# Kernel optimization log

Measured on AMD Instinct MI355X. Metric: run time of the kernel, lower is better.

The kernel has to match this reference:

```python
import jax, jax.numpy as jnp
import numpy as np

B, L, D, H = 2, 2048, 1024, 16
HD = D // H


def setup_inputs() -> dict:
    key = jax.random.key(0)
    ks = jax.random.split(key, 13)
    s = 0.02
    return {
        "x": jax.random.normal(ks[0], (B, L, D), jnp.float32),
        "pos_emb": jax.random.normal(ks[1], (1, L, D), jnp.float32),
        "Wq": jax.random.normal(ks[2], (D, D), jnp.float32) * s,
        "bq": jax.random.normal(ks[3], (D,), jnp.float32) * s,
        "Wk": jax.random.normal(ks[4], (D, D), jnp.float32) * s,
        "bk": jax.random.normal(ks[5], (D,), jnp.float32) * s,
        "Wv": jax.random.normal(ks[6], (D, D), jnp.float32) * s,
        "bv": jax.random.normal(ks[7], (D,), jnp.float32) * s,
        "Wpos": jax.random.normal(ks[8], (D, D), jnp.float32) * s,
        "pos_bias_u": jax.random.normal(ks[9], (H, HD), jnp.float32) * s,
        "pos_bias_v": jax.random.normal(ks[10], (H, HD), jnp.float32) * s,
        "Wo": jax.random.normal(ks[11], (D, D), jnp.float32) * s,
        "bo": jax.random.normal(ks[12], (D,), jnp.float32) * s,
    }


def _rel_shift(x):
    # x: (b, h, L, L) -> Transformer-XL relative shift
    b, h, q, k = x.shape
    x = jnp.pad(x, ((0, 0), (0, 0), (0, 0), (1, 0)))  # (b,h,L,L+1)
    x = x.reshape(b, h, k + 1, q)                      # (b,h,L+1,L)
    return x[:, :, 1:, :]                              # (b,h,L,L)


def reference(x, pos_emb, Wq, bq, Wk, bk, Wv, bv, Wpos, pos_bias_u, pos_bias_v, Wo, bo):
    b, seq, d = x.shape
    h, hd = pos_bias_u.shape
    scale = hd ** (-0.5)

    def proj(inp, W, bias=None):
        y = inp @ W.T
        if bias is not None:
            y = y + bias
        return y.reshape(inp.shape[0], seq, h, hd).transpose(0, 2, 1, 3)

    q = proj(x, Wq, bq)            # (b,h,L,hd)
    k = proj(x, Wk, bk)
    v = proj(x, Wv, bv)
    p = proj(pos_emb, Wpos)        # (1,h,L,hd)

    q_u = q + pos_bias_u[None, :, None, :]
    ac = jnp.einsum("bhqd,bhkd->bhqk", q_u, k)
    q_v = q + pos_bias_v[None, :, None, :]
    bd = jnp.matmul(q_v, jnp.swapaxes(p, -1, -2))  # broadcasts over batch
    bd = _rel_shift(bd)

    attn = jax.nn.softmax((ac + bd) * scale, axis=-1)
    out = jnp.einsum("bhqk,bhkd->bhqd", attn, v)
    out = out.transpose(0, 2, 1, 3).reshape(b, seq, d)
    return out @ Wo.T + bo
```

## Files before the change

### kernel.cpp

```cpp
#include <hip/hip_runtime.h>
#include <hip/hip_bf16.h>

constexpr int Lq = 2048;
constexpr int Dm = 1024;
constexpr int Hh = 16;
constexpr int HD = 64;

typedef __bf16 v8bf __attribute__((ext_vector_type(8)));
typedef short  v4s  __attribute__((ext_vector_type(4)));
typedef float  v4f  __attribute__((ext_vector_type(4)));

#define DEV static __device__ __forceinline__

DEV short f2bf(float f) {
  return (short)__builtin_bit_cast(unsigned short, __float2bfloat16(f));
}

DEV v4f MFMA(v8bf a, v8bf b, v4f c) {
  return __builtin_amdgcn_mfma_f32_16x16x32_bf16(a, b, c, 0, 0, 0);
}

template<int CTRL>
DEV float dppf(float x) {
  return __builtin_bit_cast(float, __builtin_amdgcn_update_dpp(
      0, __builtin_bit_cast(int, x), CTRL, 0xF, 0xF, true));
}
DEV float rowmax16(float x) {
  x = fmaxf(x, dppf<0xB1>(x));
  x = fmaxf(x, dppf<0x4E>(x));
  x = fmaxf(x, dppf<0x141>(x));
  x = fmaxf(x, dppf<0x140>(x));
  return x;
}
DEV float rowsum16(float x) {
  x += dppf<0xB1>(x);
  x += dppf<0x4E>(x);
  x += dppf<0x141>(x);
  x += dppf<0x140>(x);
  return x;
}

DEV float bperm(int byteaddr, float x) {
  return __builtin_bit_cast(float,
      __builtin_amdgcn_ds_bpermute(byteaddr, __builtin_bit_cast(int, x)));
}

#if __has_builtin(__builtin_amdgcn_exp2f)
DEV float exp2g(float x) { return __builtin_amdgcn_exp2f(x); }
#else
DEV float exp2g(float x) { return exp2f(x); }
#endif

DEV v4s cvt4(float4 v) {
  v4s w; w[0] = f2bf(v.x); w[1] = f2bf(v.y); w[2] = f2bf(v.z); w[3] = f2bf(v.w);
  return w;
}

template<int MODE>
__launch_bounds__(256)
__global__ void gemm_bt(const void* __restrict__ Aptr,
                        const float* __restrict__ W,
                        const float* __restrict__ bias,
                        const float* __restrict__ ubias,
                        const float* __restrict__ vbias,
                        void* __restrict__ out0,
                        void* __restrict__ out1)
{
  __shared__ short As[64][72];
  __shared__ short Bs[64][72];

  const int tid  = threadIdx.x;
  const int lane = tid & 63;
  const int wave = tid >> 6;
  const int lr   = lane & 15;
  const int lg   = lane >> 4;
  const int row0 = blockIdx.y * 64;
  const int col0 = blockIdx.x * 64;
  const int wr   = (wave >> 1) * 32;
  const int wc   = (wave & 1) * 32;

  const int srow = tid >> 2;
  const int scol = (tid & 3) * 16;

  v4f acc[2][2] = {};

  for (int k0 = 0; k0 < Dm; k0 += 64) {
    __syncthreads();
    if (MODE == 4) {
      const short* A = (const short*)Aptr;
      *(v8bf*)(&As[srow][scol]) =
          *(const v8bf*)(A + (size_t)(row0 + srow) * Dm + k0 + scol);
      *(v8bf*)(&As[srow][scol + 8]) =
          *(const v8bf*)(A + (size_t)(row0 + srow) * Dm + k0 + scol + 8);
    } else {
      const float* A = (const float*)Aptr;
      #pragma unroll
      for (int i = 0; i < 4; ++i) {
        float4 v = *(const float4*)(A + (size_t)(row0 + srow) * Dm + k0 + scol + i * 4);
        *(v4s*)(&As[srow][scol + i * 4]) = cvt4(v);
      }
    }
    #pragma unroll
    for (int i = 0; i < 4; ++i) {
      float4 v = *(const float4*)(W + (size_t)(col0 + srow) * Dm + k0 + scol + i * 4);
      *(v4s*)(&Bs[srow][scol + i * 4]) = cvt4(v);
    }
    __syncthreads();

    #pragma unroll
    for (int kk = 0; kk < 2; ++kk) {
      v8bf af[2], bfr[2];
      #pragma unroll
      for (int sm = 0; sm < 2; ++sm)
        af[sm] = *(const v8bf*)(&As[wr + sm * 16 + lr][kk * 32 + lg * 8]);
      #pragma unroll
      for (int sn = 0; sn < 2; ++sn)
        bfr[sn] = *(const v8bf*)(&Bs[wc + sn * 16 + lr][kk * 32 + lg * 8]);
      #pragma unroll
      for (int sm = 0; sm < 2; ++sm)
        #pragma unroll
        for (int sn = 0; sn < 2; ++sn)
          acc[sm][sn] = MFMA(af[sm], bfr[sn], acc[sm][sn]);
    }
  }

  #pragma unroll
  for (int sm = 0; sm < 2; ++sm) {
    #pragma unroll
    for (int sn = 0; sn < 2; ++sn) {
      #pragma unroll
      for (int r = 0; r < 4; ++r) {
        int i = row0 + wr + sm * 16 + lg * 4 + r;
        int o = col0 + wc + sn * 16 + lr;
        float val = acc[sm][sn][r];
        if (MODE == 0) {
          val += bias[o];
          int b = i >> 11, l = i & 2047;
          int h = o >> 6,  hd = o & 63;
          size_t idx = (((size_t)(b * Hh + h)) * Lq + l) * HD + hd;
          ((short*)out0)[idx] = f2bf(val + ubias[o]);
          ((short*)out1)[idx] = f2bf(val + vbias[o]);
        } else if (MODE == 1) {
          val += bias[o];
          int b = i >> 11, l = i & 2047;
          int h = o >> 6,  hd = o & 63;
          size_t idx = (((size_t)(b * Hh + h)) * Lq + l) * HD + hd;
          ((short*)out0)[idx] = f2bf(val);
        } else if (MODE == 2) {
          val += bias[o];
          int b = i >> 11, l = i & 2047;
          int h = o >> 6,  hd = o & 63;
          size_t idx = (((size_t)(b * Hh + h)) * HD + hd) * Lq + l;
          ((short*)out0)[idx] = f2bf(val);
        } else if (MODE == 3) {
          int h = o >> 6, hd = o & 63;
          size_t idx = ((size_t)h * Lq + i) * HD + hd;
          ((short*)out0)[idx] = f2bf(val);
        } else {
          ((float*)out0)[(size_t)i * Dm + o] = val + bias[o];
        }
      }
    }
  }
}

__launch_bounds__(256)
__global__ void attn_kernel(const short* __restrict__ Qu,
                            const short* __restrict__ Qv,
                            const short* __restrict__ Kb,
                            const short* __restrict__ Vt,
                            const short* __restrict__ Pb,
                            short* __restrict__ AO)
{
  __shared__ short Ks[64][72];
  __shared__ short Vs[64][72];
  __shared__ short Ps[4][16][72];

  const int tid  = threadIdx.x;
  const int lane = tid & 63;
  const int wave = tid >> 6;
  const int lr   = lane & 15;
  const int lg   = lane >> 4;
  const int bh   = blockIdx.y;
  const int h    = bh & (Hh - 1);
  const int Q0   = blockIdx.x * 64;
  const int q0   = Q0 + wave * 16;

  const short* Qu_bh = Qu + (size_t)bh * Lq * HD;
  const short* Qv_bh = Qv + (size_t)bh * Lq * HD;
  const short* Kb_bh = Kb + (size_t)bh * Lq * HD;
  const short* Vt_bh = Vt + (size_t)bh * HD * Lq;
  const short* Pb_h  = Pb + (size_t)h * Lq * HD;

  int  addr4[4];
  bool hi4[4];
  #pragma unroll
  for (int r = 0; r < 4; ++r) {
    int c = lr - (lg * 4 + r) + 15;
    hi4[r]  = (c >= 16);
    addr4[r] = (((lane & 48) | (c & 15)) << 2);
  }

  v8bf qu[2], qv1[2], qv2[2];
  {
    int q  = q0 + lr;
    int q2 = (q + 1 < Lq) ? q + 1 : Lq - 1;
    #pragma unroll
    for (int kk = 0; kk < 2; ++kk) {
      qu[kk]  = *(const v8bf*)(Qu_bh + (size_t)q  * HD + kk * 32 + lg * 8);
      qv1[kk] = *(const v8bf*)(Qv_bh + (size_t)q  * HD + kk * 32 + lg * 8);
      qv2[kk] = *(const v8bf*)(Qv_bh + (size_t)q2 * HD + kk * 32 + lg * 8);
    }
  }

  const int srow = tid >> 2;
  const int scol = (tid & 3) * 16;

  v8bf kpre0 = *(const v8bf*)(Kb_bh + (size_t)srow * HD + scol);
  v8bf kpre1 = *(const v8bf*)(Kb_bh + (size_t)srow * HD + scol + 8);
  v8bf vpre0 = *(const v8bf*)(Vt_bh + (size_t)srow * Lq + scol);
  v8bf vpre1 = *(const v8bf*)(Vt_bh + (size_t)srow * Lq + scol + 8);

  float m_r[4], l_r[4];
  v4f o_acc[4];
  #pragma unroll
  for (int r = 0; r < 4; ++r) { m_r[r] = -1e30f; l_r[r] = 0.f; }
  #pragma unroll
  for (int n = 0; n < 4; ++n) o_acc[n] = v4f{0.f, 0.f, 0.f, 0.f};

  const float sc = 0.125f * 1.44269504088896f;

  for (int ktile = 0; ktile < Lq / 64; ++ktile) {
    const int k0 = ktile * 64;
    __syncthreads();
    *(v8bf*)(&Ks[srow][scol])     = kpre0;
    *(v8bf*)(&Ks[srow][scol + 8]) = kpre1;
    *(v8bf*)(&Vs[srow][scol])     = vpre0;
    *(v8bf*)(&Vs[srow][scol + 8]) = vpre1;
    __syncthreads();
    if (ktile + 1 < Lq / 64) {
      const int kn = k0 + 64;
      kpre0 = *(const v8bf*)(Kb_bh + (size_t)(kn + srow) * HD + scol);
      kpre1 = *(const v8bf*)(Kb_bh + (size_t)(kn + srow) * HD + scol + 8);
      vpre0 = *(const v8bf*)(Vt_bh + (size_t)srow * Lq + kn + scol);
      vpre1 = *(const v8bf*)(Vt_bh + (size_t)srow * Lq + kn + scol + 8);
    }

    v4f s[4];
    #pragma unroll
    for (int kt4 = 0; kt4 < 4; ++kt4) {
      v4f a = v4f{0.f, 0.f, 0.f, 0.f};
      #pragma unroll
      for (int kk = 0; kk < 2; ++kk) {
        v8bf kb = *(const v8bf*)(&Ks[kt4 * 16 + lr][kk * 32 + lg * 8]);
        a = MFMA(qu[kk], kb, a);
      }
      s[kt4] = a;
    }

    const int thr = q0 - k0 + 15;
    const bool needT1 = (thr >= 0);
    const bool needT2 = (thr <= 76);
    const int jb1 = 2032 + k0 - q0;
    const int jb2 = k0 - q0 - 17;
    v4f t1[5] = {}, t2[5] = {};
    if (needT1) {
      #pragma unroll
      for (int n = 0; n < 5; ++n) {
        if (n * 16 <= thr) {
          int j = jb1 + n * 16 + lr;
          j = j < 0 ? 0 : (j > Lq - 1 ? Lq - 1 : j);
          v4f a = v4f{0.f, 0.f, 0.f, 0.f};
          #pragma unroll
          for (int kk = 0; kk < 2; ++kk) {
            v8bf pb = *(const v8bf*)(Pb_h + (size_t)j * HD + kk * 32 + lg * 8);
            a = MFMA(qv1[kk], pb, a);
          }
          t1[n] = a;
        }
      }
    }
    if (needT2) {
      #pragma unroll
      for (int n = 0; n < 5; ++n) {
        if (n * 16 + 15 >= thr + 2) {
          int j = jb2 + n * 16 + lr;
          j = j < 0 ? 0 : (j > Lq - 1 ? Lq - 1 : j);
          v4f a = v4f{0.f, 0.f, 0.f, 0.f};
          #pragma unroll
          for (int kk = 0; kk < 2; ++kk) {
            v8bf pb = *(const v8bf*)(Pb_h + (size_t)j * HD + kk * 32 + lg * 8);
            a = MFMA(qv2[kk], pb, a);
          }
          t2[n] = a;
        }
      }
    }

    #pragma unroll
    for (int n = 0; n < 5; ++n) {
      int cc = n * 16 + lr;
      #pragma unroll
      for (int r = 0; r < 4; ++r) {
        float v = (cc <= thr) ? t1[n][r] : ((cc == thr + 1) ? 0.f : t2[n][r]);
        t1[n][r] = v;
      }
    }

    #pragma unroll
    for (int kt4 = 0; kt4 < 4; ++kt4) {
      #pragma unroll
      for (int r = 0; r < 4; ++r) {
        float va = bperm(addr4[r], t1[kt4][r]);
        float vb = bperm(addr4[r], t1[kt4 + 1][r]);
        float bd = hi4[r] ? vb : va;
        s[kt4][r] = (s[kt4][r] + bd) * sc;
      }
    }

    #pragma unroll
    for (int r = 0; r < 4; ++r) {
      float rmax = fmaxf(fmaxf(s[0][r], s[1][r]), fmaxf(s[2][r], s[3][r]));
      rmax = rowmax16(rmax);
      float mnew  = fmaxf(m_r[r], rmax);
      float alpha = exp2g(m_r[r] - mnew);
      m_r[r] = mnew;
      float rsum = 0.f;
      #pragma unroll
      for (int kt4 = 0; kt4 < 4; ++kt4) {
        float p = exp2g(s[kt4][r] - mnew);
        s[kt4][r] = p;
        rsum += p;
      }
      rsum = rowsum16(rsum);
      l_r[r] = l_r[r] * alpha + rsum;
      #pragma unroll
      for (int n = 0; n < 4; ++n)
        o_acc[n][r] = o_acc[n][r] * alpha;
      #pragma unroll
      for (int kt4 = 0; kt4 < 4; ++kt4)
        Ps[wave][lg * 4 + r][kt4 * 16 + lr] = f2bf(s[kt4][r]);
    }
    asm volatile("s_waitcnt lgkmcnt(0)" ::: "memory");
    __builtin_amdgcn_sched_barrier(0);

    #pragma unroll
    for (int kk = 0; kk < 2; ++kk) {
      v8bf pa = *(const v8bf*)(&Ps[wave][lr][kk * 32 + lg * 8]);
      #pragma unroll
      for (int n = 0; n < 4; ++n) {
        v8bf vb = *(const v8bf*)(&Vs[n * 16 + lr][kk * 32 + lg * 8]);
        o_acc[n] = MFMA(pa, vb, o_acc[n]);
      }
    }
  }

  const int b = bh >> 4;
  #pragma unroll
  for (int r = 0; r < 4; ++r) {
    float inv = 1.0f / l_r[r];
    int q = q0 + lg * 4 + r;
    #pragma unroll
    for (int n = 0; n < 4; ++n) {
      int hd = n * 16 + lr;
      AO[((size_t)b * Lq + q) * Dm + h * HD + hd] = f2bf(o_acc[n][r] * inv);
    }
  }
}

extern "C" void kernel_launch(void* const* d_in, const int* in_sizes, int n_in,
                              void* d_out, int out_size, void* d_ws, size_t ws_size,
                              hipStream_t stream)
{
  (void)in_sizes; (void)n_in; (void)out_size; (void)ws_size;
  const float* x    = (const float*)d_in[0];
  const float* pos  = (const float*)d_in[1];
  const float* Wq   = (const float*)d_in[2];
  const float* bq   = (const float*)d_in[3];
  const float* Wk   = (const float*)d_in[4];
  const float* bk   = (const float*)d_in[5];
  const float* Wv   = (const float*)d_in[6];
  const float* bv   = (const float*)d_in[7];
  const float* Wpos = (const float*)d_in[8];
  const float* pu   = (const float*)d_in[9];
  const float* pvb  = (const float*)d_in[10];
  const float* Wo   = (const float*)d_in[11];
  const float* bo   = (const float*)d_in[12];
  float* out = (float*)d_out;

  short* Qu = (short*)d_ws;
  short* Qv = Qu + (size_t)4 * 1024 * 1024;
  short* Kb = Qv + (size_t)4 * 1024 * 1024;
  short* Vt = Kb + (size_t)4 * 1024 * 1024;
  short* Pb = Vt + (size_t)4 * 1024 * 1024;
  short* AO = Pb + (size_t)2 * 1024 * 1024;

  dim3 blk(256);
  gemm_bt<0><<<dim3(16, 64), blk, 0, stream>>>(x,   Wq,   bq,      pu,      pvb,     Qu,  Qv);
  gemm_bt<1><<<dim3(16, 64), blk, 0, stream>>>(x,   Wk,   bk,      nullptr, nullptr, Kb,  nullptr);
  gemm_bt<2><<<dim3(16, 64), blk, 0, stream>>>(x,   Wv,   bv,      nullptr, nullptr, Vt,  nullptr);
  gemm_bt<3><<<dim3(16, 32), blk, 0, stream>>>(pos, Wpos, nullptr, nullptr, nullptr, Pb,  nullptr);
  attn_kernel<<<dim3(Lq / 64, 2 * Hh), blk, 0, stream>>>(Qu, Qv, Kb, Vt, Pb, AO);
  gemm_bt<4><<<dim3(16, 64), blk, 0, stream>>>(AO,  Wo,   bo,      nullptr, nullptr, out, nullptr);
}
```

Before: 397.0 us.

## Batch QKV/pos projections into one launch, pre-convert inputs, drop LDS staging in attention

Adds kernels that convert x and pos_emb to bf16 once, then merges the four projection GEMMs into a single 3D-grid launch with per-z epilogues. The attention kernel no longer stages K/V in shared memory and reads MFMA fragments straight from global memory. It fuses the band computation into the score loop and skips the online-softmax rescale when no row max increases. This aims to cut launch count, repeated fp32 conversion of x and block-wide syncs. The cost is uncoalesced global K/V reads that rely on cache hits, plus extra conversion passes.

Result: slower. 597.5 us (+50.5%).

```diff
diff --git a/kernel.cpp b/kernel.cpp
--- a/kernel.cpp
+++ b/kernel.cpp
@@ -56,15 +56,120 @@
   return w;
 }
 
-template<int MODE>
 __launch_bounds__(256)
-__global__ void gemm_bt(const void* __restrict__ Aptr,
-                        const float* __restrict__ W,
-                        const float* __restrict__ bias,
-                        const float* __restrict__ ubias,
-                        const float* __restrict__ vbias,
-                        void* __restrict__ out0,
-                        void* __restrict__ out1)
+__global__ void cvt_bf16(const float* __restrict__ in, short* __restrict__ out,
+                         int n8)
+{
+  int i = blockIdx.x * 256 + threadIdx.x;
+  if (i >= n8) return;
+  float4 a = *(const float4*)(in + (size_t)i * 8);
+  float4 b = *(const float4*)(in + (size_t)i * 8 + 4);
+  *(v4s*)(out + (size_t)i * 8)     = cvt4(a);
+  *(v4s*)(out + (size_t)i * 8 + 4) = cvt4(b);
+}
+
+__launch_bounds__(256)
+__global__ void gemm_qkvp(const short* __restrict__ xb,
+                          const short* __restrict__ posb,
+                          const float* __restrict__ Wq, const float* __restrict__ Wk,
+                          const float* __restrict__ Wv, const float* __restrict__ Wp,
+                          const float* __restrict__ bq, const float* __restrict__ bk,
+                          const float* __restrict__ bv,
+                          const float* __restrict__ pu, const float* __restrict__ pvb,
+                          short* __restrict__ Qu, short* __restrict__ Qv,
+                          short* __restrict__ Kb, short* __restrict__ Vt,
+                          short* __restrict__ Pb)
+{
+  const int z    = blockIdx.z;
+  const int row0 = blockIdx.y * 64;
+  const int col0 = blockIdx.x * 64;
+  if (z == 3 && row0 >= Lq) return;
+  const short* A = (z == 3) ? posb : xb;
+  const float* W = (z == 0) ? Wq : (z == 1) ? Wk : (z == 2) ? Wv : Wp;
+
+  __shared__ short As[64][72];
+  __shared__ short Bs[64][72];
+
+  const int tid  = threadIdx.x;
+  const int lane = tid & 63;
+  const int wave = tid >> 6;
+  const int lr   = lane & 15;
+  const int lg   = lane >> 4;
+  const int wr   = (wave >> 1) * 32;
+  const int wc   = (wave & 1) * 32;
+  const int srow = tid >> 2;
+  const int scol = (tid & 3) * 16;
+
+  v4f acc[2][2] = {};
+
+  for (int k0 = 0; k0 < Dm; k0 += 64) {
+    __syncthreads();
+    *(v8bf*)(&As[srow][scol]) =
+        *(const v8bf*)(A + (size_t)(row0 + srow) * Dm + k0 + scol);
+    *(v8bf*)(&As[srow][scol + 8]) =
+        *(const v8bf*)(A + (size_t)(row0 + srow) * Dm + k0 + scol + 8);
+    #pragma unroll
+    for (int i = 0; i < 4; ++i) {
+      float4 v = *(const float4*)(W + (size_t)(col0 + srow) * Dm + k0 + scol + i * 4);
+      *(v4s*)(&Bs[srow][scol + i * 4]) = cvt4(v);
+    }
+    __syncthreads();
+
+    #pragma unroll
+    for (int kk = 0; kk < 2; ++kk) {
+      v8bf af[2], bfr[2];
+      #pragma unroll
+      for (int sm = 0; sm < 2; ++sm)
+        af[sm] = *(const v8bf*)(&As[wr + sm * 16 + lr][kk * 32 + lg * 8]);
+      #pragma unroll
+      for (int sn = 0; sn < 2; ++sn)
+        bfr[sn] = *(const v8bf*)(&Bs[wc + sn * 16 + lr][kk * 32 + lg * 8]);
+      #pragma unroll
+      for (int sm = 0; sm < 2; ++sm)
+        #pragma unroll
+        for (int sn = 0; sn < 2; ++sn)
+          acc[sm][sn] = MFMA(af[sm], bfr[sn], acc[sm][sn]);
+    }
+  }
+
+  #pragma unroll
+  for (int sm = 0; sm < 2; ++sm) {
+    #pragma unroll
+    for (int sn = 0; sn < 2; ++sn) {
+      #pragma unroll
+      for (int r = 0; r < 4; ++r) {
+        int i = row0 + wr + sm * 16 + lg * 4 + r;
+        int o = col0 + wc + sn * 16 + lr;
+        float val = acc[sm][sn][r];
+        int b = i >> 11, l = i & 2047;
+        int hh = o >> 6, hd = o & 63;
+        if (z == 0) {
+          val += bq[o];
+          size_t idx = (((size_t)(b * Hh + hh)) * Lq + l) * HD + hd;
+          Qu[idx] = f2bf(val + pu[o]);
+          Qv[idx] = f2bf(val + pvb[o]);
+        } else if (z == 1) {
+          val += bk[o];
+          size_t idx = (((size_t)(b * Hh + hh)) * Lq + l) * HD + hd;
+          Kb[idx] = f2bf(val);
+        } else if (z == 2) {
+          val += bv[o];
+          size_t idx = (((size_t)(b * Hh + hh)) * HD + hd) * Lq + l;
+          Vt[idx] = f2bf(val);
+        } else {
+          size_t idx = ((size_t)hh * Lq + i) * HD + hd;
+          Pb[idx] = f2bf(val);
+        }
+      }
+    }
+  }
+}
+
+__launch_bounds__(256)
+__global__ void gemm_out(const short* __restrict__ A,
+                         const float* __restrict__ W,
+                         const float* __restrict__ bias,
+                         float* __restrict__ out)
 {
   __shared__ short As[64][72];
   __shared__ short Bs[64][72];
@@ -78,7 +183,6 @@
   const int col0 = blockIdx.x * 64;
   const int wr   = (wave >> 1) * 32;
   const int wc   = (wave & 1) * 32;
-
   const int srow = tid >> 2;
   const int scol = (tid & 3) * 16;
 
@@ -86,20 +190,10 @@
 
   for (int k0 = 0; k0 < Dm; k0 += 64) {
     __syncthreads();
-    if (MODE == 4) {
-      const short* A = (const short*)Aptr;
-      *(v8bf*)(&As[srow][scol]) =
-          *(const v8bf*)(A + (size_t)(row0 + srow) * Dm + k0 + scol);
-      *(v8bf*)(&As[srow][scol + 8]) =
-          *(const v8bf*)(A + (size_t)(row0 + srow) * Dm + k0 + scol + 8);
-    } else {
-      const float* A = (const float*)Aptr;
-      #pragma unroll
-      for (int i = 0; i < 4; ++i) {
-        float4 v = *(const float4*)(A + (size_t)(row0 + srow) * Dm + k0 + scol + i * 4);
-        *(v4s*)(&As[srow][scol + i * 4]) = cvt4(v);
-      }
-    }
+    *(v8bf*)(&As[srow][scol]) =
+        *(const v8bf*)(A + (size_t)(row0 + srow) * Dm + k0 + scol);
+    *(v8bf*)(&As[srow][scol + 8]) =
+        *(const v8bf*)(A + (size_t)(row0 + srow) * Dm + k0 + scol + 8);
     #pragma unroll
     for (int i = 0; i < 4; ++i) {
       float4 v = *(const float4*)(W + (size_t)(col0 + srow) * Dm + k0 + scol + i * 4);
@@ -125,43 +219,15 @@
   }
 
   #pragma unroll
-  for (int sm = 0; sm < 2; ++sm) {
-    #pragma unroll
-    for (int sn = 0; sn < 2; ++sn) {
+  for (int sm = 0; sm < 2; ++sm)
+    #pragma unroll
+    for (int sn = 0; sn < 2; ++sn)
       #pragma unroll
       for (int r = 0; r < 4; ++r) {
         int i = row0 + wr + sm * 16 + lg * 4 + r;
         int o = col0 + wc + sn * 16 + lr;
-        float val = acc[sm][sn][r];
-        if (MODE == 0) {
-          val += bias[o];
-          int b = i >> 11, l = i & 2047;
-          int h = o >> 6,  hd = o & 63;
-          size_t idx = (((size_t)(b * Hh + h)) * Lq + l) * HD + hd;
-          ((short*)out0)[idx] = f2bf(val + ubias[o]);
-          ((short*)out1)[idx] = f2bf(val + vbias[o]);
-        } else if (MODE == 1) {
-          val += bias[o];
-          int b = i >> 11, l = i & 2047;
-          int h = o >> 6,  hd = o & 63;
-          size_t idx = (((size_t)(b * Hh + h)) * Lq + l) * HD + hd;
-          ((short*)out0)[idx] = f2bf(val);
-        } else if (MODE == 2) {
-          val += bias[o];
-          int b = i >> 11, l = i & 2047;
-          int h = o >> 6,  hd = o & 63;
-          size_t idx = (((size_t)(b * Hh + h)) * HD + hd) * Lq + l;
-          ((short*)out0)[idx] = f2bf(val);
-        } else if (MODE == 3) {
-          int h = o >> 6, hd = o & 63;
-          size_t idx = ((size_t)h * Lq + i) * HD + hd;
-          ((short*)out0)[idx] = f2bf(val);
-        } else {
-          ((float*)out0)[(size_t)i * Dm + o] = val + bias[o];
-        }
-      }
-    }
-  }
+        out[(size_t)i * Dm + o] = acc[sm][sn][r] + bias[o];
+      }
 }
 
 __launch_bounds__(256)
@@ -172,8 +238,6 @@
                             const short* __restrict__ Pb,
                             short* __restrict__ AO)
 {
-  __shared__ short Ks[64][72];
-  __shared__ short Vs[64][72];
   __shared__ short Ps[4][16][72];
 
   const int tid  = threadIdx.x;
@@ -183,21 +247,20 @@
   const int lg   = lane >> 4;
   const int bh   = blockIdx.y;
   const int h    = bh & (Hh - 1);
-  const int Q0   = blockIdx.x * 64;
-  const int q0   = Q0 + wave * 16;
+  const int q0   = blockIdx.x * 64 + wave * 16;
 
   const short* Qu_bh = Qu + (size_t)bh * Lq * HD;
   const short* Qv_bh = Qv + (size_t)bh * Lq * HD;
-  const short* Kb_bh = Kb + (size_t)bh * Lq * HD;
-  const short* Vt_bh = Vt + (size_t)bh * HD * Lq;
-  const short* Pb_h  = Pb + (size_t)h * Lq * HD;
+  const short* Kl = Kb + (size_t)bh * Lq * HD + lr * HD + lg * 8;
+  const short* Vl = Vt + (size_t)bh * HD * Lq + lr * Lq + lg * 8;
+  const short* Pl = Pb + (size_t)h * Lq * HD + lg * 8;
 
   int  addr4[4];
   bool hi4[4];
   #pragma unroll
   for (int r = 0; r < 4; ++r) {
     int c = lr - (lg * 4 + r) + 15;
-    hi4[r]  = (c >= 16);
+    hi4[r]   = (c >= 16);
     addr4[r] = (((lane & 48) | (c & 15)) << 2);
   }
 
@@ -213,14 +276,6 @@
     }
   }
 
-  const int srow = tid >> 2;
-  const int scol = (tid & 3) * 16;
-
-  v8bf kpre0 = *(const v8bf*)(Kb_bh + (size_t)srow * HD + scol);
-  v8bf kpre1 = *(const v8bf*)(Kb_bh + (size_t)srow * HD + scol + 8);
-  v8bf vpre0 = *(const v8bf*)(Vt_bh + (size_t)srow * Lq + scol);
-  v8bf vpre1 = *(const v8bf*)(Vt_bh + (size_t)srow * Lq + scol + 8);
-
   float m_r[4], l_r[4];
   v4f o_acc[4];
   #pragma unroll
@@ -230,116 +285,94 @@
 
   const float sc = 0.125f * 1.44269504088896f;
 
-  for (int ktile = 0; ktile < Lq / 64; ++ktile) {
-    const int k0 = ktile * 64;
-    __syncthreads();
-    *(v8bf*)(&Ks[srow][scol])     = kpre0;
-    *(v8bf*)(&Ks[srow][scol + 8]) = kpre1;
-    *(v8bf*)(&Vs[srow][scol])     = vpre0;
-    *(v8bf*)(&Vs[srow][scol + 8]) = vpre1;
-    __syncthreads();
-    if (ktile + 1 < Lq / 64) {
-      const int kn = k0 + 64;
-      kpre0 = *(const v8bf*)(Kb_bh + (size_t)(kn + srow) * HD + scol);
-      kpre1 = *(const v8bf*)(Kb_bh + (size_t)(kn + srow) * HD + scol + 8);
-      vpre0 = *(const v8bf*)(Vt_bh + (size_t)srow * Lq + kn + scol);
-      vpre1 = *(const v8bf*)(Vt_bh + (size_t)srow * Lq + kn + scol + 8);
-    }
-
+  for (int k0 = 0; k0 < Lq; k0 += 64) {
     v4f s[4];
     #pragma unroll
-    for (int kt4 = 0; kt4 < 4; ++kt4) {
-      v4f a = v4f{0.f, 0.f, 0.f, 0.f};
-      #pragma unroll
-      for (int kk = 0; kk < 2; ++kk) {
-        v8bf kb = *(const v8bf*)(&Ks[kt4 * 16 + lr][kk * 32 + lg * 8]);
-        a = MFMA(qu[kk], kb, a);
-      }
-      s[kt4] = a;
+    for (int kt = 0; kt < 4; ++kt) {
+      v8bf kb0 = *(const v8bf*)(Kl + (size_t)(k0 + kt * 16) * HD);
+      v8bf kb1 = *(const v8bf*)(Kl + (size_t)(k0 + kt * 16) * HD + 32);
+      v4f a = MFMA(qu[0], kb0, v4f{0.f, 0.f, 0.f, 0.f});
+      s[kt] = MFMA(qu[1], kb1, a);
     }
 
     const int thr = q0 - k0 + 15;
-    const bool needT1 = (thr >= 0);
-    const bool needT2 = (thr <= 76);
     const int jb1 = 2032 + k0 - q0;
     const int jb2 = k0 - q0 - 17;
-    v4f t1[5] = {}, t2[5] = {};
-    if (needT1) {
-      #pragma unroll
-      for (int n = 0; n < 5; ++n) {
-        if (n * 16 <= thr) {
-          int j = jb1 + n * 16 + lr;
-          j = j < 0 ? 0 : (j > Lq - 1 ? Lq - 1 : j);
-          v4f a = v4f{0.f, 0.f, 0.f, 0.f};
-          #pragma unroll
-          for (int kk = 0; kk < 2; ++kk) {
-            v8bf pb = *(const v8bf*)(Pb_h + (size_t)j * HD + kk * 32 + lg * 8);
-            a = MFMA(qv1[kk], pb, a);
-          }
-          t1[n] = a;
-        }
-      }
-    }
-    if (needT2) {
-      #pragma unroll
-      for (int n = 0; n < 5; ++n) {
-        if (n * 16 + 15 >= thr + 2) {
-          int j = jb2 + n * 16 + lr;
-          j = j < 0 ? 0 : (j > Lq - 1 ? Lq - 1 : j);
-          v4f a = v4f{0.f, 0.f, 0.f, 0.f};
-          #pragma unroll
-          for (int kk = 0; kk < 2; ++kk) {
-            v8bf pb = *(const v8bf*)(Pb_h + (size_t)j * HD + kk * 32 + lg * 8);
-            a = MFMA(qv2[kk], pb, a);
-          }
-          t2[n] = a;
-        }
-      }
-    }
-
-    #pragma unroll
-    for (int n = 0; n < 5; ++n) {
+
+    auto band = [&](int n) -> v4f {
+      v4f a1 = {0.f, 0.f, 0.f, 0.f}, a2 = {0.f, 0.f, 0.f, 0.f};
+      if (n * 16 <= thr) {
+        int j = jb1 + n * 16 + lr;
+        j = j < 0 ? 0 : (j > Lq - 1 ? Lq - 1 : j);
+        const short* p = Pl + (size_t)j * HD;
+        a1 = MFMA(qv1[0], *(const v8bf*)p, a1);
+        a1 = MFMA(qv1[1], *(const v8bf*)(p + 32), a1);
+      }
+      if (n * 16 + 15 >= thr + 2) {
+        int j = jb2 + n * 16 + lr;
+        j = j < 0 ? 0 : (j > Lq - 1 ? Lq - 1 : j);
+        const short* p = Pl + (size_t)j * HD;
+        a2 = MFMA(qv2[0], *(const v8bf*)p, a2);
+        a2 = MFMA(qv2[1], *(const v8bf*)(p + 32), a2);
+      }
       int cc = n * 16 + lr;
+      v4f t;
+      #pragma unroll
+      for (int r = 0; r < 4; ++r)
+        t[r] = (cc <= thr) ? a1[r] : ((cc == thr + 1) ? 0.f : a2[r]);
+      return t;
+    };
+
+    v4f tp = band(0);
+    #pragma unroll
+    for (int kt = 0; kt < 4; ++kt) {
+      v4f tc = band(kt + 1);
       #pragma unroll
       for (int r = 0; r < 4; ++r) {
-        float v = (cc <= thr) ? t1[n][r] : ((cc == thr + 1) ? 0.f : t2[n][r]);
-        t1[n][r] = v;
-      }
-    }
-
-    #pragma unroll
-    for (int kt4 = 0; kt4 < 4; ++kt4) {
+        float va = bperm(addr4[r], tp[r]);
+        float vb = bperm(addr4[r], tc[r]);
+        s[kt][r] = (s[kt][r] + (hi4[r] ? vb : va)) * sc;
+      }
+      tp = tc;
+    }
+
+    v8bf vf[2][4];
+    #pragma unroll
+    for (int kk = 0; kk < 2; ++kk)
+      #pragma unroll
+      for (int n = 0; n < 4; ++n)
+        vf[kk][n] = *(const v8bf*)(Vl + (size_t)n * 16 * Lq + k0 + kk * 32);
+
+    float rmax[4];
+    float need = -1e30f;
+    #pragma unroll
+    for (int r = 0; r < 4; ++r) {
+      float m0 = fmaxf(fmaxf(s[0][r], s[1][r]), fmaxf(s[2][r], s[3][r]));
+      rmax[r] = rowmax16(m0);
+      need = fmaxf(need, rmax[r] - m_r[r]);
+    }
+    if (!__all(need <= 0.f)) {
       #pragma unroll
       for (int r = 0; r < 4; ++r) {
-        float va = bperm(addr4[r], t1[kt4][r]);
-        float vb = bperm(addr4[r], t1[kt4 + 1][r]);
-        float bd = hi4[r] ? vb : va;
-        s[kt4][r] = (s[kt4][r] + bd) * sc;
-      }
-    }
-
+        float mnew  = fmaxf(m_r[r], rmax[r]);
+        float alpha = exp2g(m_r[r] - mnew);
+        m_r[r] = mnew;
+        l_r[r] *= alpha;
+        #pragma unroll
+        for (int n = 0; n < 4; ++n)
+          o_acc[n][r] *= alpha;
+      }
+    }
     #pragma unroll
     for (int r = 0; r < 4; ++r) {
-      float rmax = fmaxf(fmaxf(s[0][r], s[1][r]), fmaxf(s[2][r], s[3][r]));
-      rmax = rowmax16(rmax);
-      float mnew  = fmaxf(m_r[r], rmax);
-      float alpha = exp2g(m_r[r] - mnew);
-      m_r[r] = mnew;
       float rsum = 0.f;
       #pragma unroll
-      for (int kt4 = 0; kt4 < 4; ++kt4) {
-        float p = exp2g(s[kt4][r] - mnew);
-        s[kt4][r] = p;
+      for (int kt = 0; kt < 4; ++kt) {
+        float p = exp2g(s[kt][r] - m_r[r]);
         rsum += p;
-      }
-      rsum = rowsum16(rsum);
-      l_r[r] = l_r[r] * alpha + rsum;
-      #pragma unroll
-      for (int n = 0; n < 4; ++n)
-        o_acc[n][r] = o_acc[n][r] * alpha;
-      #pragma unroll
-      for (int kt4 = 0; kt4 < 4; ++kt4)
-        Ps[wave][lg * 4 + r][kt4 * 16 + lr] = f2bf(s[kt4][r]);
+        Ps[wave][lg * 4 + r][kt * 16 + lr] = f2bf(p);
+      }
+      l_r[r] += rowsum16(rsum);
     }
     asm volatile("s_waitcnt lgkmcnt(0)" ::: "memory");
     __builtin_amdgcn_sched_barrier(0);
@@ -348,10 +381,8 @@
     for (int kk = 0; kk < 2; ++kk) {
       v8bf pa = *(const v8bf*)(&Ps[wave][lr][kk * 32 + lg * 8]);
       #pragma unroll
-      for (int n = 0; n < 4; ++n) {
-        v8bf vb = *(const v8bf*)(&Vs[n * 16 + lr][kk * 32 + lg * 8]);
-        o_acc[n] = MFMA(pa, vb, o_acc[n]);
-      }
+      for (int n = 0; n < 4; ++n)
+        o_acc[n] = MFMA(pa, vf[kk][n], o_acc[n]);
     }
   }
 
@@ -388,18 +419,21 @@
   const float* bo   = (const float*)d_in[12];
   float* out = (float*)d_out;
 
-  short* Qu = (short*)d_ws;
-  short* Qv = Qu + (size_t)4 * 1024 * 1024;
-  short* Kb = Qv + (size_t)4 * 1024 * 1024;
-  short* Vt = Kb + (size_t)4 * 1024 * 1024;
-  short* Pb = Vt + (size_t)4 * 1024 * 1024;
-  short* AO = Pb + (size_t)2 * 1024 * 1024;
+  short* Qu   = (short*)d_ws;
+  short* Qv   = Qu   + (size_t)4 * 1024 * 1024;
+  short* Kbuf = Qv   + (size_t)4 * 1024 * 1024;
+  short* Vt   = Kbuf + (size_t)4 * 1024 * 1024;
+  short* Pb   = Vt   + (size_t)4 * 1024 * 1024;
+  short* AO   = Pb   + (size_t)2 * 1024 * 1024;
+  short* xb   = AO   + (size_t)4 * 1024 * 1024;
+  short* posb = xb   + (size_t)4 * 1024 * 1024;
 
   dim3 blk(256);
-  gemm_bt<0><<<dim3(16, 64), blk, 0, stream>>>(x,   Wq,   bq,      pu,      pvb,     Qu,  Qv);
-  gemm_bt<1><<<dim3(16, 64), blk, 0, stream>>>(x,   Wk,   bk,      nullptr, nullptr, Kb,  nullptr);
-  gemm_bt<2><<<dim3(16, 64), blk, 0, stream>>>(x,   Wv,   bv,      nullptr, nullptr, Vt,  nullptr);
-  gemm_bt<3><<<dim3(16, 32), blk, 0, stream>>>(pos, Wpos, nullptr, nullptr, nullptr, Pb,  nullptr);
-  attn_kernel<<<dim3(Lq / 64, 2 * Hh), blk, 0, stream>>>(Qu, Qv, Kb, Vt, Pb, AO);
-  gemm_bt<4><<<dim3(16, 64), blk, 0, stream>>>(AO,  Wo,   bo,      nullptr, nullptr, out, nullptr);
-}
+  cvt_bf16<<<dim3(2048), blk, 0, stream>>>(x,   xb,   524288);
+  cvt_bf16<<<dim3(1024), blk, 0, stream>>>(pos, posb, 262144);
+  gemm_qkvp<<<dim3(16, 64, 4), blk, 0, stream>>>(
+      xb, posb, Wq, Wk, Wv, Wpos, bq, bk, bv, pu, pvb,
+      Qu, Qv, Kbuf, Vt, Pb);
+  attn_kernel<<<dim3(Lq / 64, 2 * Hh), blk, 0, stream>>>(Qu, Qv, Kbuf, Vt, Pb, AO);
+  gemm_out<<<dim3(16, 64), blk, 0, stream>>>(AO, Wo, bo, out);
+}
```
